# Optimization experiments

Measured on AMD Instinct MI355X. Metric: run time of the kernel, lower is better.

Reference implementation:

```python
import jax, jax.numpy as jnp
import numpy as np

B, T, C = 4, 1024, 1024
H, K, P = 16, 31, 15  # heads, kernel_size, padding_l
R = C // H

def setup_inputs() -> dict:
    key = jax.random.key(0)
    k1, k2 = jax.random.split(key)
    x = jax.random.normal(k1, (B, T, C), dtype=jnp.float32)
    # weight_linear: nn.Linear(n_in, H*K), no bias. torch layout: (out, in)
    W = jax.random.normal(k2, (H * K, C), dtype=jnp.float32) * 0.02
    return {"x": x, "W": W}

def reference(x, W):
    # dynamic per-position filters: (B,T,H,K)
    w = jnp.einsum('btc,kc->btk', x, W).reshape(B, T, H, K)
    # weight_softmax=True, renorm_padding=False: softmax over K in fp32
    w = jax.nn.softmax(w.astype(jnp.float32), axis=-1).astype(x.dtype)
    # depthwise band conv: out[b,t,h,r] = sum_k w[b,t,h,k] * x_pad[b, t+k, h, r]
    x_pad = jnp.pad(x, ((0, 0), (P, K - 1 - P), (0, 0)))
    # windows: (B,T,C,K) -- gather of K shifted views instead of O(T^2) band matrix
    x_unf = jnp.stack([x_pad[:, k:k + T, :] for k in range(K)], axis=-1)
    x_unf = x_unf.reshape(B, T, H, R, K)
    out = jnp.einsum('bthrk,bthk->bthr', x_unf, w)
    return out.reshape(B, T, C)
```

## Files before the change

kernel.cpp:

```cpp
#include <hip/hip_runtime.h>
#include <stdint.h>

typedef __attribute__((ext_vector_type(4))) float f32x4;
typedef __attribute__((ext_vector_type(8))) short short8;
typedef __attribute__((ext_vector_type(4))) unsigned short u16x4;

#define BB 4
#define TT 1024
#define CC 1024
#define HH 16
#define KSZ 31
#define PADL 15
#define RR 64
#define NL 496
#define NP 512
#define MM 4096

__device__ __forceinline__ unsigned short f2bf(float f) {
    uint32_t u = __float_as_uint(f);
    u += 0x7FFFu + ((u >> 16) & 1u);
    return (unsigned short)(u >> 16);
}

__device__ __forceinline__ void gload_lds16(const void* g, void* l) {
    __builtin_amdgcn_global_load_lds(
        (const __attribute__((address_space(1))) unsigned int*)g,
        (__attribute__((address_space(3))) unsigned int*)l, 16, 0, 0);
}

__global__ __launch_bounds__(256) void cast_kernel(const float* __restrict__ X,
                                                   const float* __restrict__ W,
                                                   unsigned short* __restrict__ Xb,
                                                   unsigned short* __restrict__ Wb) {
    const int i = blockIdx.x * 256 + threadIdx.x;
    const int nx4 = MM * CC / 4;
    const int nw4 = NP * CC / 4;
    if (i < nx4) {
        f32x4 v = ((const f32x4*)X)[i];
        u16x4 o = { f2bf(v[0]), f2bf(v[1]), f2bf(v[2]), f2bf(v[3]) };
        ((u16x4*)Xb)[i] = o;
    } else if (i < nx4 + nw4) {
        const int j = i - nx4;
        const int n = j >> 8;
        u16x4 o = { 0, 0, 0, 0 };
        if (n < NL) {
            f32x4 v = ((const f32x4*)W)[j];
            o[0] = f2bf(v[0]); o[1] = f2bf(v[1]); o[2] = f2bf(v[2]); o[3] = f2bf(v[3]);
        }
        ((u16x4*)Wb)[j] = o;
    }
}

__global__ __launch_bounds__(256) void gemm_mfma(const unsigned short* __restrict__ Xb,
                                                 const unsigned short* __restrict__ Wb,
                                                 float* __restrict__ L) {
    __shared__ unsigned short As[64 * 64];
    __shared__ unsigned short Bs[64 * 64];

    const int tid = threadIdx.x;
    const int lane = tid & 63;
    const int wv = tid >> 6;
    const int wm = wv >> 1, wn = wv & 1;
    const int m0 = blockIdx.y * 64, n0 = blockIdx.x * 64;

    f32x4 acc[2][2] = {};

    for (int kt = 0; kt < CC / 64; ++kt) {
        const int k0 = kt * 64;
#pragma unroll
        for (int p = 0; p < 2; ++p) {
            const int c = p * 256 + tid;
            const int row = c >> 3, kcs = c & 7;
            const int kg = (kcs ^ (row & 7)) << 3;
            gload_lds16(Xb + (size_t)(m0 + row) * CC + k0 + kg, (char*)As + c * 16);
            gload_lds16(Wb + (size_t)(n0 + row) * CC + k0 + kg, (char*)Bs + c * 16);
        }
        __syncthreads();
#pragma unroll
        for (int ks = 0; ks < 2; ++ks) {
            short8 af[2], bfv[2];
            const int kc = ks * 4 + (lane >> 4);
#pragma unroll
            for (int s = 0; s < 2; ++s) {
                const int ra = wm * 32 + s * 16 + (lane & 15);
                af[s] = *(const short8*)((const char*)As + ra * 128 + ((kc ^ (ra & 7)) << 4));
                const int rb = wn * 32 + s * 16 + (lane & 15);
                bfv[s] = *(const short8*)((const char*)Bs + rb * 128 + ((kc ^ (rb & 7)) << 4));
            }
#pragma unroll
            for (int si = 0; si < 2; ++si)
#pragma unroll
                for (int sj = 0; sj < 2; ++sj)
                    acc[si][sj] = __builtin_amdgcn_mfma_f32_16x16x32_bf16(
                        af[si], bfv[sj], acc[si][sj], 0, 0, 0);
        }
        __syncthreads();
    }

    const int col = lane & 15, rbase = (lane >> 4) * 4;
#pragma unroll
    for (int si = 0; si < 2; ++si)
#pragma unroll
        for (int sj = 0; sj < 2; ++sj) {
            const int n = n0 + wn * 32 + sj * 16 + col;
            if (n < NL) {
#pragma unroll
                for (int r = 0; r < 4; ++r) {
                    const int m = m0 + wm * 32 + si * 16 + rbase + r;
                    L[(size_t)m * NL + n] = acc[si][sj][r];
                }
            }
        }
}

__global__ __launch_bounds__(256) void softmax_kernel(const float* __restrict__ L,
                                                      float* __restrict__ wq) {
    const int g = blockIdx.x * 256 + threadIdx.x;
    const int m = g >> 4, h = g & 15;
    const float* lp = L + (size_t)m * NL + h * KSZ;
    float lv[KSZ];
    float mx = -1e30f;
#pragma unroll
    for (int k = 0; k < KSZ; ++k) { lv[k] = lp[k]; mx = fmaxf(mx, lv[k]); }
    float s = 0.f;
#pragma unroll
    for (int k = 0; k < KSZ; ++k) { lv[k] = __expf(lv[k] - mx); s += lv[k]; }
    const float inv = 1.f / s;
    f32x4* op = (f32x4*)(wq + (size_t)g * 32);
#pragma unroll
    for (int q = 0; q < 8; ++q) {
        f32x4 o;
#pragma unroll
        for (int j = 0; j < 4; ++j) {
            const int k = q * 4 + j;
            o[j] = (k < KSZ) ? lv[k] * inv : 0.f;
        }
        op[q] = o;
    }
}

__global__ __launch_bounds__(256) void conv_kernel(const float* __restrict__ X,
                                                   const float* __restrict__ wq,
                                                   float* __restrict__ out) {
    __shared__ float xsT[64 * 96];

    const int tid = threadIdx.x, lane = tid & 63, wv = tid >> 6;
    int bid = blockIdx.x;
    const int tt = bid & 15;
    const int h = (bid >> 4) & 15;
    const int b = bid >> 8;
    const int t0 = tt * 64;

    for (int i = 0; i < 24; ++i) {
        const int row = i * 4 + wv;
        const int tg = t0 - PADL + row;
        float v = 0.f;
        if (row < 94 && tg >= 0 && tg < TT)
            v = X[(size_t)(b * TT + tg) * CC + h * RR + lane];
        const int tc = row >> 2;
        *(float*)((char*)xsT + lane * 384 + ((tc ^ (lane & 7)) << 4) + (row & 3) * 4) = v;
    }
    __syncthreads();

#pragma unroll
    for (int g = 0; g < 2; ++g) {
        const int gl = wv * 16 + g * 8;
        f32x4 xw[10];
#pragma unroll
        for (int q = 0; q < 10; ++q) {
            const int tc = (gl >> 2) + q;
            xw[q] = *(const f32x4*)((const char*)xsT + lane * 384 + ((tc ^ (lane & 7)) << 4));
        }
        float acc[8] = {};
#pragma unroll
        for (int tl = 0; tl < 8; ++tl) {
            const f32x4* wp = (const f32x4*)(wq +
                (size_t)((b * TT + t0 + gl + tl) * HH + h) * 32);
#pragma unroll
            for (int kq = 0; kq < 8; ++kq) {
                const f32x4 w4 = wp[kq];
#pragma unroll
                for (int j = 0; j < 4; ++j) {
                    const int e = tl + kq * 4 + j;
                    acc[tl] = fmaf(w4[j], xw[e >> 2][e & 3], acc[tl]);
                }
            }
        }
#pragma unroll
        for (int tl = 0; tl < 8; ++tl)
            out[(size_t)(b * TT + t0 + gl + tl) * CC + h * RR + lane] = acc[tl];
    }
}

extern "C" void kernel_launch(void* const* d_in, const int* in_sizes, int n_in,
                              void* d_out, int out_size, void* d_ws, size_t ws_size,
                              hipStream_t stream) {
    const float* x = (const float*)d_in[0];
    const float* W = (const float*)d_in[1];
    float* out = (float*)d_out;
    char* ws = (char*)d_ws;

    unsigned short* Xb = (unsigned short*)ws;
    unsigned short* Wb = (unsigned short*)(ws + (size_t)MM * CC * 2);
    float* L = (float*)d_out;
    float* wq = (float*)ws;

    cast_kernel<<<(MM * CC / 4 + NP * CC / 4 + 255) / 256, 256, 0, stream>>>(x, W, Xb, Wb);
    gemm_mfma<<<dim3(NP / 64, MM / 64), 256, 0, stream>>>(Xb, Wb, L);
    softmax_kernel<<<MM * HH / 256, 256, 0, stream>>>(L, wq);
    conv_kernel<<<BB * HH * (TT / 64), 256, 0, stream>>>(x, wq, out);
}
```

Measured before the change: 115.5 us.

## Fuse softmax into conv kernel, double-buffer GEMM, store logits transposed

Removes the separate softmax kernel and computes the per-position softmax inside the conv kernel, reading logits from shared memory. The GEMM now writes the logits transposed (head-tap major) as vector stores so the conv blocks can load them coalesced. It also double-buffers its LDS tiles, prefetching the next K-tile while the current one is computed, and remaps block indices. This saves one launch and the round trip of the padded softmax weights through global memory, at the cost of more shared memory per conv block and larger GEMM LDS use.

```diff
diff --git a/kernel.cpp b/kernel.cpp
--- a/kernel.cpp
+++ b/kernel.cpp
@@ -53,29 +53,44 @@
 
 __global__ __launch_bounds__(256) void gemm_mfma(const unsigned short* __restrict__ Xb,
                                                  const unsigned short* __restrict__ Wb,
-                                                 float* __restrict__ L) {
-    __shared__ unsigned short As[64 * 64];
-    __shared__ unsigned short Bs[64 * 64];
+                                                 float* __restrict__ LT) {
+    __shared__ unsigned short As[2 * 64 * 64];
+    __shared__ unsigned short Bs[2 * 64 * 64];
 
     const int tid = threadIdx.x;
     const int lane = tid & 63;
     const int wv = tid >> 6;
     const int wm = wv >> 1, wn = wv & 1;
-    const int m0 = blockIdx.y * 64, n0 = blockIdx.x * 64;
+
+    int bid = blockIdx.x;
+    bid = (bid & 7) * 64 + (bid >> 3);
+    const int n0 = (bid & 7) * 64;
+    const int m0 = (bid >> 3) * 64;
 
     f32x4 acc[2][2] = {};
 
+#define STAGE(ktt, bufsel) do {                                                  \
+        const int k0s = (ktt) * 64;                                              \
+        _Pragma("unroll")                                                        \
+        for (int p = 0; p < 2; ++p) {                                            \
+            const int c = p * 256 + tid;                                         \
+            const int row = c >> 3, kcs = c & 7;                                 \
+            const int kg = (kcs ^ (row & 7)) << 3;                               \
+            gload_lds16(Xb + (size_t)(m0 + row) * CC + k0s + kg,                 \
+                        (char*)As + (bufsel) * 8192 + c * 16);                   \
+            gload_lds16(Wb + (size_t)(n0 + row) * CC + k0s + kg,                 \
+                        (char*)Bs + (bufsel) * 8192 + c * 16);                   \
+        }                                                                        \
+    } while (0)
+
+    int cur = 0;
+    STAGE(0, 0);
+    __syncthreads();
+
     for (int kt = 0; kt < CC / 64; ++kt) {
-        const int k0 = kt * 64;
-#pragma unroll
-        for (int p = 0; p < 2; ++p) {
-            const int c = p * 256 + tid;
-            const int row = c >> 3, kcs = c & 7;
-            const int kg = (kcs ^ (row & 7)) << 3;
-            gload_lds16(Xb + (size_t)(m0 + row) * CC + k0 + kg, (char*)As + c * 16);
-            gload_lds16(Wb + (size_t)(n0 + row) * CC + k0 + kg, (char*)Bs + c * 16);
-        }
-        __syncthreads();
+        if (kt + 1 < CC / 64) STAGE(kt + 1, cur ^ 1);
+        const char* Ab = (const char*)As + cur * 8192;
+        const char* Bb = (const char*)Bs + cur * 8192;
 #pragma unroll
         for (int ks = 0; ks < 2; ++ks) {
             short8 af[2], bfv[2];
@@ -83,9 +98,9 @@
 #pragma unroll
             for (int s = 0; s < 2; ++s) {
                 const int ra = wm * 32 + s * 16 + (lane & 15);
-                af[s] = *(const short8*)((const char*)As + ra * 128 + ((kc ^ (ra & 7)) << 4));
+                af[s] = *(const short8*)(Ab + ra * 128 + ((kc ^ (ra & 7)) << 4));
                 const int rb = wn * 32 + s * 16 + (lane & 15);
-                bfv[s] = *(const short8*)((const char*)Bs + rb * 128 + ((kc ^ (rb & 7)) << 4));
+                bfv[s] = *(const short8*)(Bb + rb * 128 + ((kc ^ (rb & 7)) << 4));
             }
 #pragma unroll
             for (int si = 0; si < 2; ++si)
@@ -95,7 +110,9 @@
                         af[si], bfv[sj], acc[si][sj], 0, 0, 0);
         }
         __syncthreads();
-    }
+        cur ^= 1;
+    }
+#undef STAGE
 
     const int col = lane & 15, rbase = (lane >> 4) * 4;
 #pragma unroll
@@ -104,45 +121,18 @@
         for (int sj = 0; sj < 2; ++sj) {
             const int n = n0 + wn * 32 + sj * 16 + col;
             if (n < NL) {
-#pragma unroll
-                for (int r = 0; r < 4; ++r) {
-                    const int m = m0 + wm * 32 + si * 16 + rbase + r;
-                    L[(size_t)m * NL + n] = acc[si][sj][r];
-                }
+                const int m = m0 + wm * 32 + si * 16 + rbase;
+                *(f32x4*)&LT[(size_t)n * MM + m] = acc[si][sj];
             }
         }
 }
 
-__global__ __launch_bounds__(256) void softmax_kernel(const float* __restrict__ L,
-                                                      float* __restrict__ wq) {
-    const int g = blockIdx.x * 256 + threadIdx.x;
-    const int m = g >> 4, h = g & 15;
-    const float* lp = L + (size_t)m * NL + h * KSZ;
-    float lv[KSZ];
-    float mx = -1e30f;
-#pragma unroll
-    for (int k = 0; k < KSZ; ++k) { lv[k] = lp[k]; mx = fmaxf(mx, lv[k]); }
-    float s = 0.f;
-#pragma unroll
-    for (int k = 0; k < KSZ; ++k) { lv[k] = __expf(lv[k] - mx); s += lv[k]; }
-    const float inv = 1.f / s;
-    f32x4* op = (f32x4*)(wq + (size_t)g * 32);
-#pragma unroll
-    for (int q = 0; q < 8; ++q) {
-        f32x4 o;
-#pragma unroll
-        for (int j = 0; j < 4; ++j) {
-            const int k = q * 4 + j;
-            o[j] = (k < KSZ) ? lv[k] * inv : 0.f;
-        }
-        op[q] = o;
-    }
-}
-
-__global__ __launch_bounds__(256) void conv_kernel(const float* __restrict__ X,
-                                                   const float* __restrict__ wq,
-                                                   float* __restrict__ out) {
-    __shared__ float xsT[64 * 96];
+__global__ __launch_bounds__(256) void conv_fused(const float* __restrict__ X,
+                                                  const float* __restrict__ LT,
+                                                  float* __restrict__ out) {
+    __shared__ float xsT[64 * 100];
+    __shared__ float lsm[32 * 64];
+    __shared__ float wsm[64 * 36];
 
     const int tid = threadIdx.x, lane = tid & 63, wv = tid >> 6;
     int bid = blockIdx.x;
@@ -158,7 +148,37 @@
         if (row < 94 && tg >= 0 && tg < TT)
             v = X[(size_t)(b * TT + tg) * CC + h * RR + lane];
         const int tc = row >> 2;
-        *(float*)((char*)xsT + lane * 384 + ((tc ^ (lane & 7)) << 4) + (row & 3) * 4) = v;
+        xsT[lane * 100 + ((tc ^ (lane & 7)) << 2) + (row & 3)] = v;
+    }
+#pragma unroll
+    for (int i = 0; i < 8; ++i) {
+        const int kk = wv * 8 + i;
+        if (kk < KSZ)
+            lsm[kk * 64 + lane] = LT[(size_t)(h * KSZ + kk) * MM + b * TT + t0 + lane];
+    }
+    __syncthreads();
+
+    {
+        const int j = lane & 3, tl = wv * 16 + (lane >> 2);
+        float v[8];
+        float mx = -1e30f;
+#pragma unroll
+        for (int i = 0; i < 8; ++i) {
+            const int kk = j * 8 + i;
+            v[i] = (kk < KSZ) ? lsm[kk * 64 + tl] : -1e30f;
+            mx = fmaxf(mx, v[i]);
+        }
+        mx = fmaxf(mx, __shfl_xor(mx, 1));
+        mx = fmaxf(mx, __shfl_xor(mx, 2));
+        float s = 0.f;
+#pragma unroll
+        for (int i = 0; i < 8; ++i) { v[i] = __expf(v[i] - mx); s += v[i]; }
+        s += __shfl_xor(s, 1);
+        s += __shfl_xor(s, 2);
+        const float inv = 1.f / s;
+#pragma unroll
+        for (int i = 0; i < 8; ++i)
+            wsm[tl * 36 + j * 8 + i] = v[i] * inv;
     }
     __syncthreads();
 
@@ -169,26 +189,25 @@
 #pragma unroll
         for (int q = 0; q < 10; ++q) {
             const int tc = (gl >> 2) + q;
-            xw[q] = *(const f32x4*)((const char*)xsT + lane * 384 + ((tc ^ (lane & 7)) << 4));
+            xw[q] = *(const f32x4*)&xsT[lane * 100 + ((tc ^ (lane & 7)) << 2)];
         }
         float acc[8] = {};
 #pragma unroll
-        for (int tl = 0; tl < 8; ++tl) {
-            const f32x4* wp = (const f32x4*)(wq +
-                (size_t)((b * TT + t0 + gl + tl) * HH + h) * 32);
+        for (int tl8 = 0; tl8 < 8; ++tl8) {
+            const float* wp = &wsm[(gl + tl8) * 36];
 #pragma unroll
             for (int kq = 0; kq < 8; ++kq) {
-                const f32x4 w4 = wp[kq];
-#pragma unroll
-                for (int j = 0; j < 4; ++j) {
-                    const int e = tl + kq * 4 + j;
-                    acc[tl] = fmaf(w4[j], xw[e >> 2][e & 3], acc[tl]);
+                const f32x4 w4 = *(const f32x4*)(wp + kq * 4);
+#pragma unroll
+                for (int jj = 0; jj < 4; ++jj) {
+                    const int e = tl8 + kq * 4 + jj;
+                    acc[tl8] = fmaf(w4[jj], xw[e >> 2][e & 3], acc[tl8]);
                 }
             }
         }
 #pragma unroll
-        for (int tl = 0; tl < 8; ++tl)
-            out[(size_t)(b * TT + t0 + gl + tl) * CC + h * RR + lane] = acc[tl];
+        for (int tl8 = 0; tl8 < 8; ++tl8)
+            out[(size_t)(b * TT + t0 + gl + tl8) * CC + h * RR + lane] = acc[tl8];
     }
 }
 
@@ -201,12 +220,10 @@
     char* ws = (char*)d_ws;
 
     unsigned short* Xb = (unsigned short*)ws;
-    unsigned short* Wb = (unsigned short*)(ws + (size_t)MM * CC * 2);
-    float* L = (float*)d_out;
-    float* wq = (float*)ws;
+    unsigned short* Wb = (unsigned short*)(ws + 8388608);
+    float* LT = (float*)(ws + 9437184);
 
     cast_kernel<<<(MM * CC / 4 + NP * CC / 4 + 255) / 256, 256, 0, stream>>>(x, W, Xb, Wb);
-    gemm_mfma<<<dim3(NP / 64, MM / 64), 256, 0, stream>>>(Xb, Wb, L);
-    softmax_kernel<<<MM * HH / 256, 256, 0, stream>>>(L, wq);
-    conv_kernel<<<BB * HH * (TT / 64), 256, 0, stream>>>(x, wq, out);
-}
+    gemm_mfma<<<NP / 64 * (MM / 64), 256, 0, stream>>>(Xb, Wb, LT);
+    conv_fused<<<BB * HH * (TT / 64), 256, 0, stream>>>(x, LT, out);
+}
```

Result: faster. 111.9 us (-3.1%).
